# Kernel optimization log

Measured on AMD Instinct MI355X. Metric: run time of the kernel, lower is better.

## Reference

```python
import jax, jax.numpy as jnp
import numpy as np

B, S, D, H = 2, 2048, 1024, 16
DK = D // H


def setup_inputs() -> dict:
    key = jax.random.key(0)
    ks = jax.random.split(key, 11)
    def lin(k):
        kw, kb = jax.random.split(k)
        bound = 1.0 / np.sqrt(D)
        w = jax.random.uniform(kw, (D, D), jnp.float32, -bound, bound)
        b = jax.random.uniform(kb, (D,), jnp.float32, -bound, bound)
        return w, b
    wq_w, wq_b = lin(ks[0])
    wk_w, wk_b = lin(ks[1])
    wv_w, wv_b = lin(ks[2])
    wo_w, wo_b = lin(ks[3])
    q = jax.random.normal(ks[4], (B, S, D), jnp.float32)
    k = jax.random.normal(ks[5], (B, S, D), jnp.float32)
    v = jax.random.normal(ks[6], (B, S, D), jnp.float32)
    # causal mask, broadcastable to (B, H, S, S); 0 -> masked
    mask = jnp.tril(jnp.ones((S, S), jnp.int32))[None, None, :, :]
    return {"q": q, "k": k, "v": v, "mask": mask,
            "wq_w": wq_w, "wq_b": wq_b, "wk_w": wk_w, "wk_b": wk_b,
            "wv_w": wv_w, "wv_b": wv_b, "wo_w": wo_w, "wo_b": wo_b}


def reference(q, k, v, mask, wq_w, wq_b, wk_w, wk_b, wv_w, wv_b, wo_w, wo_b):
    # projections (torch Linear: x @ W^T + b)
    def split_heads(x):  # (B,S,D) -> (B,H,S,DK)
        return x.reshape(B, S, H, DK).transpose(0, 2, 1, 3)
    Q = split_heads(q @ wq_w.T + wq_b)
    K = split_heads(k @ wk_w.T + wk_b)
    V = split_heads(v @ wv_w.T + wv_b)
    scores = jnp.einsum('bhqd,bhkd->bhqk', Q, K) / np.sqrt(DK).astype(np.float32)
    scores = jnp.where(mask == 0, jnp.float32(-1e9), scores)
    attn = jax.nn.softmax(scores, axis=-1)
    out = jnp.einsum('bhqk,bhkd->bhqd', attn, V)  # (B,H,S,DK)
    out = out.transpose(0, 2, 1, 3).reshape(B, S, D)
    return out @ wo_w.T + wo_b
```

## Files before the change

### kernel.cpp

```cpp
#include <hip/hip_runtime.h>

#define DEV __device__ __forceinline__

typedef __attribute__((ext_vector_type(8))) short short8;
typedef __attribute__((ext_vector_type(4))) float f32x4;
typedef __attribute__((ext_vector_type(4))) unsigned int u32x4;
typedef __bf16 bf16x8 __attribute__((ext_vector_type(8)));
typedef unsigned int u32;
typedef unsigned short u16;

constexpr int Bb = 2, Ss = 2048, Dd = 1024, Hh = 16, DKc = 64;
constexpr int Kk = 1024;

#define QSCALE 0.1803368801111204f

DEV u16 f2bf(float f) {
  u32 u = __builtin_bit_cast(u32, f);
  u32 r = (u + 0x7fffu + ((u >> 16) & 1u)) >> 16;
  return (u16)r;
}

DEV u32 pk_bf16(float lo, float hi) {
  u32 w;
  asm("v_cvt_pk_bf16_f32 %0, %1, %2" : "=v"(w) : "v"(lo), "v"(hi));
  return w;
}

DEV f32x4 mfma16(short8 a, short8 b, f32x4 c) {
  return __builtin_amdgcn_mfma_f32_16x16x32_bf16(
      __builtin_bit_cast(bf16x8, a), __builtin_bit_cast(bf16x8, b), c, 0, 0, 0);
}

DEV void gload_lds16(const u16* g, u16* lds) {
  __builtin_amdgcn_global_load_lds(
      (const __attribute__((address_space(1))) u32*)g,
      (__attribute__((address_space(3))) u32*)lds, 16, 0, 0);
}

struct CvtArgs {
  const float* in[4];
  u16* out[4];
  int n[4];
};

__global__ __launch_bounds__(256) void cvt_all(CvtArgs a) {
  int z = blockIdx.z;
  int i = (blockIdx.x * 256 + threadIdx.x) * 4;
  if (i >= a.n[z]) return;
  float4 v = *reinterpret_cast<const float4*>(a.in[z] + i);
  ushort4 o;
  o.x = f2bf(v.x); o.y = f2bf(v.y); o.z = f2bf(v.z); o.w = f2bf(v.w);
  *reinterpret_cast<ushort4*>(a.out[z] + i) = o;
}

template<int MT, int NT>
DEV void gemm_core(const u16* __restrict__ A, const u16* __restrict__ Bt,
                   u16* smA, u16* smB, f32x4 (&acc)[MT][NT], int gm0, int gn0) {
  constexpr int NSTEP = Kk / 32;
  constexpr int SA = MT * 1024;
  constexpr int SB = NT * 1024;
  constexpr int S = MT / 2 + NT / 2;
  const int tid = threadIdx.x;
  const int w = tid >> 6, l = tid & 63;
  const int g = (l >> 4) & 3, r = l & 15;
  const int wm = w >> 1, wn = w & 1;
  const int srow = l >> 2, scol = (l & 3) * 8;

  auto stage = [&](int buf, int kt) {
    int kb = kt * 32;
#pragma unroll
    for (int cc = 0; cc < MT / 2; ++cc) {
      int c = w + cc * 4;
      gload_lds16(A + (size_t)(gm0 + c * 16 + srow) * Kk + kb + scol,
                  smA + buf * SA + c * 512);
    }
#pragma unroll
    for (int cc = 0; cc < NT / 2; ++cc) {
      int c = w + cc * 4;
      gload_lds16(Bt + (size_t)(gn0 + c * 16 + srow) * Kk + kb + scol,
                  smB + buf * SB + c * 512);
    }
  };

  stage(0, 0);
  stage(1, 1);
  for (int kt = 0; kt < NSTEP; ++kt) {
    const int buf = kt % 3;
    if (kt + 1 < NSTEP) {
      if constexpr (S == 4) asm volatile("s_waitcnt vmcnt(4)" ::: "memory");
      else                  asm volatile("s_waitcnt vmcnt(3)" ::: "memory");
    } else {
      asm volatile("s_waitcnt vmcnt(0)" ::: "memory");
    }
    __builtin_amdgcn_s_barrier();
    __builtin_amdgcn_sched_barrier(0);
    if (kt + 2 < NSTEP) stage((kt + 2) % 3, kt + 2);

    short8 af[MT], bf_[NT];
#pragma unroll
    for (int t = 0; t < MT; ++t)
      af[t] = *reinterpret_cast<const short8*>(
          smA + buf * SA + (wm * (MT * 16) + t * 16 + r) * 32 + g * 8);
#pragma unroll
    for (int t = 0; t < NT; ++t)
      bf_[t] = *reinterpret_cast<const short8*>(
          smB + buf * SB + (wn * (NT * 16) + t * 16 + r) * 32 + g * 8);
    __builtin_amdgcn_s_setprio(1);
#pragma unroll
    for (int mt = 0; mt < MT; ++mt)
#pragma unroll
      for (int nt = 0; nt < NT; ++nt)
        acc[mt][nt] = mfma16(af[mt], bf_[nt], acc[mt][nt]);
    __builtin_amdgcn_s_setprio(0);
  }
}

template<int MT, int NT>
DEV void gemm_core_mix(const float* __restrict__ A, const u16* __restrict__ Bt,
                       u16* smA, u16* smB, f32x4 (&acc)[MT][NT], int gm0, int gn0) {
  constexpr int NSTEP = Kk / 32;
  constexpr int SA = MT * 1024, SB = NT * 1024;
  const int tid = threadIdx.x;
  const int w = tid >> 6, l = tid & 63;
  const int g = (l >> 4) & 3, r = l & 15;
  const int wm = w >> 1, wn = w & 1;
  const int srow = l >> 2, scol = (l & 3) * 8;

  float4 a0[MT / 2][2], a1[MT / 2][2];

  auto loadA = [&](float4 (&dst)[MT / 2][2], int kt) {
    int kb = kt * 32;
#pragma unroll
    for (int c = 0; c < MT / 2; ++c) {
      int p = tid + c * 256;
      const float* src = A + (size_t)(gm0 + (p >> 2)) * Kk + kb + (p & 3) * 8;
      dst[c][0] = *reinterpret_cast<const float4*>(src);
      dst[c][1] = *reinterpret_cast<const float4*>(src + 4);
    }
  };
  auto writeA = [&](float4 (&s)[MT / 2][2], int buf) {
#pragma unroll
    for (int c = 0; c < MT / 2; ++c) {
      int p = tid + c * 256;
      u32x4 wv;
      wv.x = pk_bf16(s[c][0].x, s[c][0].y);
      wv.y = pk_bf16(s[c][0].z, s[c][0].w);
      wv.z = pk_bf16(s[c][1].x, s[c][1].y);
      wv.w = pk_bf16(s[c][1].z, s[c][1].w);
      *reinterpret_cast<u32x4*>(smA + buf * SA + p * 8) = wv;
    }
  };
  auto stageB = [&](int buf, int kt) {
    int kb = kt * 32;
#pragma unroll
    for (int cc = 0; cc < NT / 2; ++cc) {
      int c = w + cc * 4;
      gload_lds16(Bt + (size_t)(gn0 + c * 16 + srow) * Kk + kb + scol,
                  smB + buf * SB + c * 512);
    }
  };

  loadA(a0, 0); stageB(0, 0);
  loadA(a1, 1); stageB(1, 1);
  for (int kt = 0; kt < NSTEP; ++kt) {
    const int bufA = kt & 1, bufB = kt % 3;
    if (kt & 1) { writeA(a1, bufA); if (kt + 2 < NSTEP) loadA(a1, kt + 2); }
    else        { writeA(a0, bufA); if (kt + 2 < NSTEP) loadA(a0, kt + 2); }
    if (kt + 2 < NSTEP)      asm volatile("s_waitcnt vmcnt(10)" ::: "memory");
    else if (kt + 1 < NSTEP) asm volatile("s_waitcnt vmcnt(6)" ::: "memory");
    else                     asm volatile("s_waitcnt vmcnt(0)" ::: "memory");
    asm volatile("s_waitcnt lgkmcnt(0)" ::: "memory");
    __builtin_amdgcn_s_barrier();
    __builtin_amdgcn_sched_barrier(0);
    if (kt + 2 < NSTEP) stageB((kt + 2) % 3, kt + 2);

    short8 af[MT], bf_[NT];
#pragma unroll
    for (int t = 0; t < MT; ++t)
      af[t] = *reinterpret_cast<const short8*>(
          smA + bufA * SA + (wm * (MT * 16) + t * 16 + r) * 32 + g * 8);
#pragma unroll
    for (int t = 0; t < NT; ++t)
      bf_[t] = *reinterpret_cast<const short8*>(
          smB + bufB * SB + (wn * (NT * 16) + t * 16 + r) * 32 + g * 8);
    __builtin_amdgcn_s_setprio(1);
#pragma unroll
    for (int mt = 0; mt < MT; ++mt)
#pragma unroll
      for (int nt = 0; nt < NT; ++nt)
        acc[mt][nt] = mfma16(af[mt], bf_[nt], acc[mt][nt]);
    __builtin_amdgcn_s_setprio(0);
  }
}

__global__ __launch_bounds__(256, 3) void proj_qkv(
    const float* __restrict__ xq, const float* __restrict__ xk, const float* __restrict__ xv,
    const u16* __restrict__ Wq, const u16* __restrict__ Wk, const u16* __restrict__ Wv,
    const float* __restrict__ bq, const float* __restrict__ bk, const float* __restrict__ bv,
    u16* __restrict__ Qh, u16* __restrict__ Kh, u16* __restrict__ Vt) {
  __shared__ u16 smA[2 * 4096], smB[3 * 4096];
  const int flat = (blockIdx.z * 32 + blockIdx.y) * 8 + blockIdx.x;
  const int zby = (flat & 7) * 12 + ((flat >> 3) % 12);
  const int bx = flat / 96;
  const int z = zby >> 5, by = zby & 31;
  const float* A = z == 0 ? xq : (z == 1 ? xk : xv);
  const u16* W = z == 0 ? Wq : (z == 1 ? Wk : Wv);
  const float* bias = z == 0 ? bq : (z == 1 ? bk : bv);
  u16* out = z == 0 ? Qh : (z == 1 ? Kh : Vt);
  const float sc = z == 0 ? QSCALE : 1.0f;
  const int gm0 = by * 128, gn0 = bx * 128;
  f32x4 acc[4][4] = {};
  gemm_core_mix<4, 4>(A, W, smA, smB, acc, gm0, gn0);

  const int tid = threadIdx.x;
  const int w = tid >> 6, l = tid & 63, g = (l >> 4) & 3, r = l & 15;
  const int wm = w >> 1, wn = w & 1;
#pragma unroll
  for (int mt = 0; mt < 4; ++mt) {
#pragma unroll
    for (int nt = 0; nt < 4; ++nt) {
      int ncol = gn0 + wn * 64 + nt * 16 + r;
      int h = ncol >> 6, dk = ncol & 63;
      float bb = bias[ncol];
      int mrow0 = gm0 + wm * 64 + mt * 16 + g * 4;
      int b = mrow0 >> 11, s0 = mrow0 & 2047;
      if (z < 2) {
#pragma unroll
        for (int i = 0; i < 4; ++i)
          out[(((size_t)b * Hh + h) * Ss + s0 + i) * DKc + dk] =
              f2bf((acc[mt][nt][i] + bb) * sc);
      } else {
        ushort4 ov;
        ov.x = f2bf(acc[mt][nt][0] + bb);
        ov.y = f2bf(acc[mt][nt][1] + bb);
        ov.z = f2bf(acc[mt][nt][2] + bb);
        ov.w = f2bf(acc[mt][nt][3] + bb);
        *reinterpret_cast<ushort4*>(
            &out[(((size_t)b * Hh + h) * DKc + dk) * Ss + s0]) = ov;
      }
    }
  }
}

__global__ __launch_bounds__(256, 2) void attn(
    const u16* __restrict__ Qh, const u16* __restrict__ Kh,
    const u16* __restrict__ Vt, u16* __restrict__ Ob) {
  __shared__ u16 smK[4][64 * 64];
  __shared__ u16 smV[4][64 * 64];
  __shared__ u16 smP[4][16 * 72];

  const int fid = blockIdx.y * 16 + blockIdx.x;
  const int xcd = fid & 7, slot = fid >> 3;
  const int bh = xcd * 4 + (slot >> 4);
  const int pair = slot & 15;
  const int bidx = bh >> 4, h = bh & 15;

  const int tid = threadIdx.x, w = tid >> 6, l = tid & 63;
  const int g = (l >> 4) & 3, r = l & 15;

  const u16* Qb = Qh + (size_t)bh * Ss * DKc;
  const u16* Kb = Kh + (size_t)bh * Ss * DKc;
  const u16* Vb = Vt + (size_t)bh * DKc * Ss;
  u16* Pw = smP[w];

  const int srow0 = tid >> 3, schunk = tid & 7;

  auto stage = [&](int sl, int kb) {
#pragma unroll
    for (int j = 0; j < 2; ++j) {
      int row = j * 32 + srow0;
      int c = schunk ^ (row & 7);
      u16* dK = smK[sl] + (j * 256 + w * 64) * 8;
      u16* dV = smV[sl] + (j * 256 + w * 64) * 8;
      gload_lds16(Kb + (size_t)(kb + row) * DKc + c * 8, dK);
      gload_lds16(Vb + (size_t)row * Ss + kb + c * 8, dV);
    }
  };

  for (int t2 = 0; t2 < 2; ++t2) {
    const int qt = (t2 == 0) ? (31 - pair) : pair;
    const int ntile = qt + 1;
    const int npair = (ntile + 1) >> 1;
    const int qw = qt * 64 + w * 16;
    const int q = qw + r;

    if (t2) __builtin_amdgcn_s_barrier();

    short8 qf[2];
    qf[0] = *reinterpret_cast<const short8*>(Qb + (size_t)q * DKc + g * 8);
    qf[1] = *reinterpret_cast<const short8*>(Qb + (size_t)q * DKc + 32 + g * 8);

    stage(0, 0);
    if (ntile > 1) stage(1, 64);

    f32x4 o[4] = {};
    float m_s = -3e38f, l_s = 0.f;

    for (int pp = 0; pp < npair; ++pp) {
      const int slotA = (pp & 1) * 2;
      const int kbA = pp * 128;
      const bool hasB = (2 * pp + 1 < ntile);
      const bool diagA = (2 * pp == qt);
      const bool diagB = hasB && (2 * pp + 1 == qt);

      asm volatile("s_waitcnt vmcnt(0)" ::: "memory");
      __builtin_amdgcn_s_barrier();
      __builtin_amdgcn_sched_barrier(0);
      if (pp + 1 < npair) {
        int nb = ((pp + 1) & 1) * 2;
        stage(nb, kbA + 128);
        if (2 * pp + 3 < ntile) stage(nb + 1, kbA + 192);
      }

      f32x4 sA[4] = {}, sB[4] = {};
      __builtin_amdgcn_s_setprio(1);
#pragma unroll
      for (int ks = 0; ks < 2; ++ks)
#pragma unroll
        for (int nt = 0; nt < 4; ++nt) {
          int row = nt * 16 + r;
          int ch = (ks * 4 + g) ^ (row & 7);
          short8 kf = *reinterpret_cast<const short8*>(&smK[slotA][row * 64 + ch * 8]);
          sA[nt] = mfma16(kf, qf[ks], sA[nt]);
        }
      if (hasB) {
#pragma unroll
        for (int ks = 0; ks < 2; ++ks)
#pragma unroll
          for (int nt = 0; nt < 4; ++nt) {
            int row = nt * 16 + r;
            int ch = (ks * 4 + g) ^ (row & 7);
            short8 kf = *reinterpret_cast<const short8*>(&smK[slotA + 1][row * 64 + ch * 8]);
            sB[nt] = mfma16(kf, qf[ks], sB[nt]);
          }
      }
      __builtin_amdgcn_s_setprio(0);

      const int qloc = w * 16 + r;
      if (diagA) {
#pragma unroll
        for (int nt = 0; nt < 4; ++nt)
#pragma unroll
          for (int i = 0; i < 4; ++i)
            if (nt * 16 + g * 4 + i > qloc) sA[nt][i] = -1e30f;
      }
      if (diagB) {
#pragma unroll
        for (int nt = 0; nt < 4; ++nt)
#pragma unroll
          for (int i = 0; i < 4; ++i)
            if (nt * 16 + g * 4 + i > qloc) sB[nt][i] = -1e30f;
      }

      float mx0 = fmaxf(fmaxf(sA[0][0], sA[0][1]), fmaxf(sA[0][2], sA[0][3]));
      float mx1 = fmaxf(fmaxf(sA[1][0], sA[1][1]), fmaxf(sA[1][2], sA[1][3]));
      float mx2 = fmaxf(fmaxf(sA[2][0], sA[2][1]), fmaxf(sA[2][2], sA[2][3]));
      float mx3 = fmaxf(fmaxf(sA[3][0], sA[3][1]), fmaxf(sA[3][2], sA[3][3]));
      float mx = fmaxf(fmaxf(mx0, mx1), fmaxf(mx2, mx3));
      if (hasB) {
        float nx0 = fmaxf(fmaxf(sB[0][0], sB[0][1]), fmaxf(sB[0][2], sB[0][3]));
        float nx1 = fmaxf(fmaxf(sB[1][0], sB[1][1]), fmaxf(sB[1][2], sB[1][3]));
        float nx2 = fmaxf(fmaxf(sB[2][0], sB[2][1]), fmaxf(sB[2][2], sB[2][3]));
        float nx3 = fmaxf(fmaxf(sB[3][0], sB[3][1]), fmaxf(sB[3][2], sB[3][3]));
        mx = fmaxf(mx, fmaxf(fmaxf(nx0, nx1), fmaxf(nx2, nx3)));
      }

      if (__any(mx > m_s + 8.f)) {
        float mr = fmaxf(mx, __shfl_xor(mx, 16));
        mr = fmaxf(mr, __shfl_xor(mr, 32));
        float mn = fmaxf(m_s, mr);
        float f = __builtin_amdgcn_exp2f(m_s - mn);
        m_s = mn;
        l_s *= f;
#pragma unroll
        for (int dt = 0; dt < 4; ++dt) {
          o[dt][0] *= f; o[dt][1] *= f; o[dt][2] *= f; o[dt][3] *= f;
        }
      }

#pragma unroll
      for (int nt = 0; nt < 4; ++nt) {
        float p0 = __builtin_amdgcn_exp2f(sA[nt][0] - m_s);
        float p1 = __builtin_amdgcn_exp2f(sA[nt][1] - m_s);
        float p2 = __builtin_amdgcn_exp2f(sA[nt][2] - m_s);
        float p3 = __builtin_amdgcn_exp2f(sA[nt][3] - m_s);
        l_s += (p0 + p1) + (p2 + p3);
        *reinterpret_cast<u32*>(&Pw[r * 72 + nt * 16 + g * 4])     = pk_bf16(p0, p1);
        *reinterpret_cast<u32*>(&Pw[r * 72 + nt * 16 + g * 4 + 2]) = pk_bf16(p2, p3);
      }
      __builtin_amdgcn_s_setprio(1);
#pragma unroll
      for (int ks = 0; ks < 2; ++ks) {
        short8 pf = *reinterpret_cast<const short8*>(&Pw[r * 72 + ks * 32 + g * 8]);
#pragma unroll
        for (int dt = 0; dt < 4; ++dt) {
          int row = dt * 16 + r;
          int ch = (ks * 4 + g) ^ (row & 7);
          short8 vf = *reinterpret_cast<const short8*>(&smV[slotA][row * 64 + ch * 8]);
          o[dt] = mfma16(vf, pf, o[dt]);
        }
      }
      __builtin_amdgcn_s_setprio(0);

      if (hasB) {
#pragma unroll
        for (int nt = 0; nt < 4; ++nt) {
          float p0 = __builtin_amdgcn_exp2f(sB[nt][0] - m_s);
          float p1 = __builtin_amdgcn_exp2f(sB[nt][1] - m_s);
          float p2 = __builtin_amdgcn_exp2f(sB[nt][2] - m_s);
          float p3 = __builtin_amdgcn_exp2f(sB[nt][3] - m_s);
          l_s += (p0 + p1) + (p2 + p3);
          *reinterpret_cast<u32*>(&Pw[r * 72 + nt * 16 + g * 4])     = pk_bf16(p0, p1);
          *reinterpret_cast<u32*>(&Pw[r * 72 + nt * 16 + g * 4 + 2]) = pk_bf16(p2, p3);
        }
        __builtin_amdgcn_s_setprio(1);
#pragma unroll
        for (int ks = 0; ks < 2; ++ks) {
          short8 pf = *reinterpret_cast<const short8*>(&Pw[r * 72 + ks * 32 + g * 8]);
#pragma unroll
          for (int dt = 0; dt < 4; ++dt) {
            int row = dt * 16 + r;
            int ch = (ks * 4 + g) ^ (row & 7);
            short8 vf = *reinterpret_cast<const short8*>(&smV[slotA + 1][row * 64 + ch * 8]);
            o[dt] = mfma16(vf, pf, o[dt]);
          }
        }
        __builtin_amdgcn_s_setprio(0);
      }
    }

    float lt = l_s;
    lt += __shfl_xor(lt, 16);
    lt += __shfl_xor(lt, 32);
    float inv = 1.f / lt;
    size_t ro = ((size_t)bidx * Ss + q) * Dd + h * DKc;
#pragma unroll
    for (int dt = 0; dt < 4; ++dt) {
      ushort4 ov;
      ov.x = f2bf(o[dt][0] * inv);
      ov.y = f2bf(o[dt][1] * inv);
      ov.z = f2bf(o[dt][2] * inv);
      ov.w = f2bf(o[dt][3] * inv);
      *reinterpret_cast<ushort4*>(&Ob[ro + dt * 16 + g * 4]) = ov;
    }
  }
}

__global__ __launch_bounds__(256, 2) void gemm_out(
    const u16* __restrict__ Ob, const u16* __restrict__ Wo,
    const float* __restrict__ bo, float* __restrict__ out) {
  __shared__ u16 smA[3 * 64 * 32], smB[3 * 128 * 32];
  const int flat = blockIdx.y * 8 + blockIdx.x;
  const int by = (flat & 7) * 8 + ((flat >> 3) & 7);
  const int bx = flat >> 6;
  const int gm0 = by * 64, gn0 = bx * 128;
  f32x4 acc[2][4] = {};
  gemm_core<2, 4>(Ob, Wo, smA, smB, acc, gm0, gn0);

  const int tid = threadIdx.x;
  const int w = tid >> 6, l = tid & 63, g = (l >> 4) & 3, r = l & 15;
  const int wm = w >> 1, wn = w & 1;
#pragma unroll
  for (int mt = 0; mt < 2; ++mt) {
#pragma unroll
    for (int nt = 0; nt < 4; ++nt) {
      int ncol = gn0 + wn * 64 + nt * 16 + r;
      float bb = bo[ncol];
#pragma unroll
      for (int i = 0; i < 4; ++i) {
        int mrow = gm0 + wm * 32 + mt * 16 + g * 4 + i;
        out[(size_t)mrow * Dd + ncol] = acc[mt][nt][i] + bb;
      }
    }
  }
}

extern "C" void kernel_launch(void* const* d_in, const int* in_sizes, int n_in,
                              void* d_out, int out_size, void* d_ws, size_t ws_size,
                              hipStream_t stream) {
  const float* q    = (const float*)d_in[0];
  const float* k    = (const float*)d_in[1];
  const float* v    = (const float*)d_in[2];
  const float* wq_w = (const float*)d_in[4];
  const float* wq_b = (const float*)d_in[5];
  const float* wk_w = (const float*)d_in[6];
  const float* wk_b = (const float*)d_in[7];
  const float* wv_w = (const float*)d_in[8];
  const float* wv_b = (const float*)d_in[9];
  const float* wo_w = (const float*)d_in[10];
  const float* wo_b = (const float*)d_in[11];

  char* ws = (char*)d_ws;
  u16* Wqb = (u16*)(ws + 25165824);
  u16* Wkb = (u16*)(ws + 27262976);
  u16* Wvb = (u16*)(ws + 29360128);
  u16* Wob = (u16*)(ws + 31457280);
  u16* Qh  = (u16*)(ws + 33554432);
  u16* Kh  = (u16*)(ws + 41943040);
  u16* Vt  = (u16*)(ws + 50331648);
  u16* Ob  = (u16*)(ws + 0);

  CvtArgs ca;
  ca.in[0] = wq_w; ca.out[0] = Wqb; ca.n[0] = 1048576;
  ca.in[1] = wk_w; ca.out[1] = Wkb; ca.n[1] = 1048576;
  ca.in[2] = wv_w; ca.out[2] = Wvb; ca.n[2] = 1048576;
  ca.in[3] = wo_w; ca.out[3] = Wob; ca.n[3] = 1048576;

  cvt_all<<<dim3(1024, 1, 4), 256, 0, stream>>>(ca);
  proj_qkv<<<dim3(8, 32, 3), 256, 0, stream>>>(q, k, v, Wqb, Wkb, Wvb,
                                               wq_b, wk_b, wv_b, Qh, Kh, Vt);
  attn<<<dim3(16, 32), 256, 0, stream>>>(Qh, Kh, Vt, Ob);
  gemm_out<<<dim3(8, 64), 256, 0, stream>>>(Ob, Wob, wo_b, (float*)d_out);
}
```

Measured before the change: 109.5 us.

## Split K/V staging, one q-tile per block, unroll GEMM loop by two

The attention kernel now gives each block a single query tile, launches twice as many blocks ordered heaviest first, and drops the paired heavy/light tile balancing and the XCD-aware block mapping. K and V use separate double buffers, so the next K tiles load while softmax and PV run and V is refetched after PV. Shared memory is smaller and launch bounds go to 3 blocks per CU. The padded P stride changes from 72 to 76. The GEMM core loop is unrolled by two with the A register write moved between fragment loads and MFMAs to overlap LDS writes with compute. This risks load imbalance from causal tile sizes and more barriers per iteration.

```diff
diff --git a/kernel.cpp b/kernel.cpp
--- a/kernel.cpp
+++ b/kernel.cpp
@@ -159,37 +159,53 @@
                   smB + buf * SB + c * 512);
     }
   };
+  auto frags = [&](int bufA, int bufB, short8 (&af)[MT], short8 (&bf_)[NT]) {
+#pragma unroll
+    for (int t = 0; t < MT; ++t)
+      af[t] = *reinterpret_cast<const short8*>(
+          smA + bufA * SA + (wm * (MT * 16) + t * 16 + r) * 32 + g * 8);
+#pragma unroll
+    for (int t = 0; t < NT; ++t)
+      bf_[t] = *reinterpret_cast<const short8*>(
+          smB + bufB * SB + (wn * (NT * 16) + t * 16 + r) * 32 + g * 8);
+  };
+  auto mma = [&](short8 (&af)[MT], short8 (&bf_)[NT]) {
+    __builtin_amdgcn_s_setprio(1);
+#pragma unroll
+    for (int mt = 0; mt < MT; ++mt)
+#pragma unroll
+      for (int nt = 0; nt < NT; ++nt)
+        acc[mt][nt] = mfma16(af[mt], bf_[nt], acc[mt][nt]);
+    __builtin_amdgcn_s_setprio(0);
+  };
 
   loadA(a0, 0); stageB(0, 0);
   loadA(a1, 1); stageB(1, 1);
-  for (int kt = 0; kt < NSTEP; ++kt) {
-    const int bufA = kt & 1, bufB = kt % 3;
-    if (kt & 1) { writeA(a1, bufA); if (kt + 2 < NSTEP) loadA(a1, kt + 2); }
-    else        { writeA(a0, bufA); if (kt + 2 < NSTEP) loadA(a0, kt + 2); }
-    if (kt + 2 < NSTEP)      asm volatile("s_waitcnt vmcnt(10)" ::: "memory");
-    else if (kt + 1 < NSTEP) asm volatile("s_waitcnt vmcnt(6)" ::: "memory");
-    else                     asm volatile("s_waitcnt vmcnt(0)" ::: "memory");
+  writeA(a0, 0);
+
+  for (int kt = 0; kt < NSTEP; kt += 2) {
+    asm volatile("s_waitcnt vmcnt(10)" ::: "memory");
     asm volatile("s_waitcnt lgkmcnt(0)" ::: "memory");
     __builtin_amdgcn_s_barrier();
     __builtin_amdgcn_sched_barrier(0);
-    if (kt + 2 < NSTEP) stageB((kt + 2) % 3, kt + 2);
-
-    short8 af[MT], bf_[NT];
-#pragma unroll
-    for (int t = 0; t < MT; ++t)
-      af[t] = *reinterpret_cast<const short8*>(
-          smA + bufA * SA + (wm * (MT * 16) + t * 16 + r) * 32 + g * 8);
-#pragma unroll
-    for (int t = 0; t < NT; ++t)
-      bf_[t] = *reinterpret_cast<const short8*>(
-          smB + bufB * SB + (wn * (NT * 16) + t * 16 + r) * 32 + g * 8);
-    __builtin_amdgcn_s_setprio(1);
-#pragma unroll
-    for (int mt = 0; mt < MT; ++mt)
-#pragma unroll
-      for (int nt = 0; nt < NT; ++nt)
-        acc[mt][nt] = mfma16(af[mt], bf_[nt], acc[mt][nt]);
-    __builtin_amdgcn_s_setprio(0);
+    if (kt + 2 < NSTEP) { stageB((kt + 2) % 3, kt + 2); loadA(a0, kt + 2); }
+    {
+      short8 af[MT], bf_[NT];
+      frags(0, kt % 3, af, bf_);
+      writeA(a1, 1);
+      mma(af, bf_);
+    }
+    asm volatile("s_waitcnt vmcnt(10)" ::: "memory");
+    asm volatile("s_waitcnt lgkmcnt(0)" ::: "memory");
+    __builtin_amdgcn_s_barrier();
+    __builtin_amdgcn_sched_barrier(0);
+    if (kt + 3 < NSTEP) { stageB((kt + 3) % 3, kt + 3); loadA(a1, kt + 3); }
+    {
+      short8 af[MT], bf_[NT];
+      frags(1, (kt + 1) % 3, af, bf_);
+      if (kt + 2 < NSTEP) writeA(a0, 0);
+      mma(af, bf_);
+    }
   }
 }
 
@@ -242,17 +258,15 @@
   }
 }
 
-__global__ __launch_bounds__(256, 2) void attn(
+__global__ __launch_bounds__(256, 3) void attn(
     const u16* __restrict__ Qh, const u16* __restrict__ Kh,
     const u16* __restrict__ Vt, u16* __restrict__ Ob) {
-  __shared__ u16 smK[4][64 * 64];
-  __shared__ u16 smV[4][64 * 64];
-  __shared__ u16 smP[4][16 * 72];
-
-  const int fid = blockIdx.y * 16 + blockIdx.x;
-  const int xcd = fid & 7, slot = fid >> 3;
-  const int bh = xcd * 4 + (slot >> 4);
-  const int pair = slot & 15;
+  __shared__ u16 smK[2][64 * 64];
+  __shared__ u16 smV[2][64 * 64];
+  __shared__ u16 smP[4][16 * 76];
+
+  const int bh = blockIdx.x;
+  const int qt = 31 - blockIdx.y;
   const int bidx = bh >> 4, h = bh & 15;
 
   const int tid = threadIdx.x, w = tid >> 6, l = tid & 63;
@@ -265,184 +279,199 @@
 
   const int srow0 = tid >> 3, schunk = tid & 7;
 
-  auto stage = [&](int sl, int kb) {
+  auto stageK = [&](int sl, int kb) {
 #pragma unroll
     for (int j = 0; j < 2; ++j) {
       int row = j * 32 + srow0;
       int c = schunk ^ (row & 7);
-      u16* dK = smK[sl] + (j * 256 + w * 64) * 8;
-      u16* dV = smV[sl] + (j * 256 + w * 64) * 8;
-      gload_lds16(Kb + (size_t)(kb + row) * DKc + c * 8, dK);
-      gload_lds16(Vb + (size_t)row * Ss + kb + c * 8, dV);
-    }
-  };
-
-  for (int t2 = 0; t2 < 2; ++t2) {
-    const int qt = (t2 == 0) ? (31 - pair) : pair;
-    const int ntile = qt + 1;
-    const int npair = (ntile + 1) >> 1;
-    const int qw = qt * 64 + w * 16;
-    const int q = qw + r;
-
-    if (t2) __builtin_amdgcn_s_barrier();
-
-    short8 qf[2];
-    qf[0] = *reinterpret_cast<const short8*>(Qb + (size_t)q * DKc + g * 8);
-    qf[1] = *reinterpret_cast<const short8*>(Qb + (size_t)q * DKc + 32 + g * 8);
-
-    stage(0, 0);
-    if (ntile > 1) stage(1, 64);
-
-    f32x4 o[4] = {};
-    float m_s = -3e38f, l_s = 0.f;
-
-    for (int pp = 0; pp < npair; ++pp) {
-      const int slotA = (pp & 1) * 2;
-      const int kbA = pp * 128;
-      const bool hasB = (2 * pp + 1 < ntile);
-      const bool diagA = (2 * pp == qt);
-      const bool diagB = hasB && (2 * pp + 1 == qt);
-
-      asm volatile("s_waitcnt vmcnt(0)" ::: "memory");
-      __builtin_amdgcn_s_barrier();
-      __builtin_amdgcn_sched_barrier(0);
-      if (pp + 1 < npair) {
-        int nb = ((pp + 1) & 1) * 2;
-        stage(nb, kbA + 128);
-        if (2 * pp + 3 < ntile) stage(nb + 1, kbA + 192);
-      }
-
-      f32x4 sA[4] = {}, sB[4] = {};
-      __builtin_amdgcn_s_setprio(1);
+      gload_lds16(Kb + (size_t)(kb + row) * DKc + c * 8,
+                  smK[sl] + (j * 256 + w * 64) * 8);
+    }
+  };
+  auto stageV = [&](int sl, int kb) {
+#pragma unroll
+    for (int j = 0; j < 2; ++j) {
+      int row = j * 32 + srow0;
+      int c = schunk ^ (row & 7);
+      gload_lds16(Vb + (size_t)row * Ss + kb + c * 8,
+                  smV[sl] + (j * 256 + w * 64) * 8);
+    }
+  };
+
+  const int ntile = qt + 1;
+  const int npair = (ntile + 1) >> 1;
+  const int qw = qt * 64 + w * 16;
+  const int q = qw + r;
+
+  short8 qf[2];
+  qf[0] = *reinterpret_cast<const short8*>(Qb + (size_t)q * DKc + g * 8);
+  qf[1] = *reinterpret_cast<const short8*>(Qb + (size_t)q * DKc + 32 + g * 8);
+
+  {
+    int kb1 = (ntile > 1) ? 64 : 0;
+    stageK(0, 0); stageK(1, kb1);
+    stageV(0, 0); stageV(1, kb1);
+  }
+
+  f32x4 o[4] = {};
+  float m_s = -3e38f, l_s = 0.f;
+
+  for (int pp = 0; pp < npair; ++pp) {
+    const int kbA = pp * 128;
+    const bool hasB = (2 * pp + 1 < ntile);
+    const bool diagA = (2 * pp == qt);
+    const bool diagB = hasB && (2 * pp + 1 == qt);
+
+    asm volatile("s_waitcnt vmcnt(4)" ::: "memory");
+    __builtin_amdgcn_s_barrier();
+    __builtin_amdgcn_sched_barrier(0);
+
+    f32x4 sA[4] = {}, sB[4] = {};
+    __builtin_amdgcn_s_setprio(1);
+#pragma unroll
+    for (int ks = 0; ks < 2; ++ks)
+#pragma unroll
+      for (int nt = 0; nt < 4; ++nt) {
+        int row = nt * 16 + r;
+        int ch = (ks * 4 + g) ^ (row & 7);
+        short8 kf = *reinterpret_cast<const short8*>(&smK[0][row * 64 + ch * 8]);
+        sA[nt] = mfma16(kf, qf[ks], sA[nt]);
+      }
+    if (hasB) {
 #pragma unroll
       for (int ks = 0; ks < 2; ++ks)
 #pragma unroll
         for (int nt = 0; nt < 4; ++nt) {
           int row = nt * 16 + r;
           int ch = (ks * 4 + g) ^ (row & 7);
-          short8 kf = *reinterpret_cast<const short8*>(&smK[slotA][row * 64 + ch * 8]);
-          sA[nt] = mfma16(kf, qf[ks], sA[nt]);
+          short8 kf = *reinterpret_cast<const short8*>(&smK[1][row * 64 + ch * 8]);
+          sB[nt] = mfma16(kf, qf[ks], sB[nt]);
         }
-      if (hasB) {
-#pragma unroll
-        for (int ks = 0; ks < 2; ++ks)
-#pragma unroll
-          for (int nt = 0; nt < 4; ++nt) {
-            int row = nt * 16 + r;
-            int ch = (ks * 4 + g) ^ (row & 7);
-            short8 kf = *reinterpret_cast<const short8*>(&smK[slotA + 1][row * 64 + ch * 8]);
-            sB[nt] = mfma16(kf, qf[ks], sB[nt]);
-          }
-      }
-      __builtin_amdgcn_s_setprio(0);
-
-      const int qloc = w * 16 + r;
-      if (diagA) {
-#pragma unroll
-        for (int nt = 0; nt < 4; ++nt)
-#pragma unroll
-          for (int i = 0; i < 4; ++i)
-            if (nt * 16 + g * 4 + i > qloc) sA[nt][i] = -1e30f;
-      }
-      if (diagB) {
-#pragma unroll
-        for (int nt = 0; nt < 4; ++nt)
-#pragma unroll
-          for (int i = 0; i < 4; ++i)
-            if (nt * 16 + g * 4 + i > qloc) sB[nt][i] = -1e30f;
-      }
-
-      float mx0 = fmaxf(fmaxf(sA[0][0], sA[0][1]), fmaxf(sA[0][2], sA[0][3]));
-      float mx1 = fmaxf(fmaxf(sA[1][0], sA[1][1]), fmaxf(sA[1][2], sA[1][3]));
-      float mx2 = fmaxf(fmaxf(sA[2][0], sA[2][1]), fmaxf(sA[2][2], sA[2][3]));
-      float mx3 = fmaxf(fmaxf(sA[3][0], sA[3][1]), fmaxf(sA[3][2], sA[3][3]));
-      float mx = fmaxf(fmaxf(mx0, mx1), fmaxf(mx2, mx3));
-      if (hasB) {
-        float nx0 = fmaxf(fmaxf(sB[0][0], sB[0][1]), fmaxf(sB[0][2], sB[0][3]));
-        float nx1 = fmaxf(fmaxf(sB[1][0], sB[1][1]), fmaxf(sB[1][2], sB[1][3]));
-        float nx2 = fmaxf(fmaxf(sB[2][0], sB[2][1]), fmaxf(sB[2][2], sB[2][3]));
-        float nx3 = fmaxf(fmaxf(sB[3][0], sB[3][1]), fmaxf(sB[3][2], sB[3][3]));
-        mx = fmaxf(mx, fmaxf(fmaxf(nx0, nx1), fmaxf(nx2, nx3)));
-      }
-
-      if (__any(mx > m_s + 8.f)) {
-        float mr = fmaxf(mx, __shfl_xor(mx, 16));
-        mr = fmaxf(mr, __shfl_xor(mr, 32));
-        float mn = fmaxf(m_s, mr);
-        float f = __builtin_amdgcn_exp2f(m_s - mn);
-        m_s = mn;
-        l_s *= f;
-#pragma unroll
-        for (int dt = 0; dt < 4; ++dt) {
-          o[dt][0] *= f; o[dt][1] *= f; o[dt][2] *= f; o[dt][3] *= f;
-        }
-      }
-
+    }
+    __builtin_amdgcn_s_setprio(0);
+
+    asm volatile("s_waitcnt vmcnt(0)" ::: "memory");
+    __builtin_amdgcn_s_barrier();
+    __builtin_amdgcn_sched_barrier(0);
+    if (pp + 1 < npair) {
+      int nkb = kbA + 128;
+      int nkb1 = (2 * pp + 3 < ntile) ? nkb + 64 : nkb;
+      stageK(0, nkb); stageK(1, nkb1);
+    }
+
+    const int qloc = w * 16 + r;
+    if (diagA) {
+#pragma unroll
+      for (int nt = 0; nt < 4; ++nt)
+#pragma unroll
+        for (int i = 0; i < 4; ++i)
+          if (nt * 16 + g * 4 + i > qloc) sA[nt][i] = -1e30f;
+    }
+    if (diagB) {
+#pragma unroll
+      for (int nt = 0; nt < 4; ++nt)
+#pragma unroll
+        for (int i = 0; i < 4; ++i)
+          if (nt * 16 + g * 4 + i > qloc) sB[nt][i] = -1e30f;
+    }
+
+    float mx0 = fmaxf(fmaxf(sA[0][0], sA[0][1]), fmaxf(sA[0][2], sA[0][3]));
+    float mx1 = fmaxf(fmaxf(sA[1][0], sA[1][1]), fmaxf(sA[1][2], sA[1][3]));
+    float mx2 = fmaxf(fmaxf(sA[2][0], sA[2][1]), fmaxf(sA[2][2], sA[2][3]));
+    float mx3 = fmaxf(fmaxf(sA[3][0], sA[3][1]), fmaxf(sA[3][2], sA[3][3]));
+    float mx = fmaxf(fmaxf(mx0, mx1), fmaxf(mx2, mx3));
+    if (hasB) {
+      float nx0 = fmaxf(fmaxf(sB[0][0], sB[0][1]), fmaxf(sB[0][2], sB[0][3]));
+      float nx1 = fmaxf(fmaxf(sB[1][0], sB[1][1]), fmaxf(sB[1][2], sB[1][3]));
+      float nx2 = fmaxf(fmaxf(sB[2][0], sB[2][1]), fmaxf(sB[2][2], sB[2][3]));
+      float nx3 = fmaxf(fmaxf(sB[3][0], sB[3][1]), fmaxf(sB[3][2], sB[3][3]));
+      mx = fmaxf(mx, fmaxf(fmaxf(nx0, nx1), fmaxf(nx2, nx3)));
+    }
+
+    if (__any(mx > m_s + 8.f)) {
+      float mr = fmaxf(mx, __shfl_xor(mx, 16));
+      mr = fmaxf(mr, __shfl_xor(mr, 32));
+      float mn = fmaxf(m_s, mr);
+      float f = __builtin_amdgcn_exp2f(m_s - mn);
+      m_s = mn;
+      l_s *= f;
+#pragma unroll
+      for (int dt = 0; dt < 4; ++dt) {
+        o[dt][0] *= f; o[dt][1] *= f; o[dt][2] *= f; o[dt][3] *= f;
+      }
+    }
+
+#pragma unroll
+    for (int nt = 0; nt < 4; ++nt) {
+      float p0 = __builtin_amdgcn_exp2f(sA[nt][0] - m_s);
+      float p1 = __builtin_amdgcn_exp2f(sA[nt][1] - m_s);
+      float p2 = __builtin_amdgcn_exp2f(sA[nt][2] - m_s);
+      float p3 = __builtin_amdgcn_exp2f(sA[nt][3] - m_s);
+      l_s += (p0 + p1) + (p2 + p3);
+      *reinterpret_cast<u32*>(&Pw[r * 76 + nt * 16 + g * 4])     = pk_bf16(p0, p1);
+      *reinterpret_cast<u32*>(&Pw[r * 76 + nt * 16 + g * 4 + 2]) = pk_bf16(p2, p3);
+    }
+    __builtin_amdgcn_s_setprio(1);
+#pragma unroll
+    for (int ks = 0; ks < 2; ++ks) {
+      short8 pf = *reinterpret_cast<const short8*>(&Pw[r * 76 + ks * 32 + g * 8]);
+#pragma unroll
+      for (int dt = 0; dt < 4; ++dt) {
+        int row = dt * 16 + r;
+        int ch = (ks * 4 + g) ^ (row & 7);
+        short8 vf = *reinterpret_cast<const short8*>(&smV[0][row * 64 + ch * 8]);
+        o[dt] = mfma16(vf, pf, o[dt]);
+      }
+    }
+    __builtin_amdgcn_s_setprio(0);
+
+    if (hasB) {
 #pragma unroll
       for (int nt = 0; nt < 4; ++nt) {
-        float p0 = __builtin_amdgcn_exp2f(sA[nt][0] - m_s);
-        float p1 = __builtin_amdgcn_exp2f(sA[nt][1] - m_s);
-        float p2 = __builtin_amdgcn_exp2f(sA[nt][2] - m_s);
-        float p3 = __builtin_amdgcn_exp2f(sA[nt][3] - m_s);
+        float p0 = __builtin_amdgcn_exp2f(sB[nt][0] - m_s);
+        float p1 = __builtin_amdgcn_exp2f(sB[nt][1] - m_s);
+        float p2 = __builtin_amdgcn_exp2f(sB[nt][2] - m_s);
+        float p3 = __builtin_amdgcn_exp2f(sB[nt][3] - m_s);
         l_s += (p0 + p1) + (p2 + p3);
-        *reinterpret_cast<u32*>(&Pw[r * 72 + nt * 16 + g * 4])     = pk_bf16(p0, p1);
-        *reinterpret_cast<u32*>(&Pw[r * 72 + nt * 16 + g * 4 + 2]) = pk_bf16(p2, p3);
+        *reinterpret_cast<u32*>(&Pw[r * 76 + nt * 16 + g * 4])     = pk_bf16(p0, p1);
+        *reinterpret_cast<u32*>(&Pw[r * 76 + nt * 16 + g * 4 + 2]) = pk_bf16(p2, p3);
       }
       __builtin_amdgcn_s_setprio(1);
 #pragma unroll
       for (int ks = 0; ks < 2; ++ks) {
-        short8 pf = *reinterpret_cast<const short8*>(&Pw[r * 72 + ks * 32 + g * 8]);
+        short8 pf = *reinterpret_cast<const short8*>(&Pw[r * 76 + ks * 32 + g * 8]);
 #pragma unroll
         for (int dt = 0; dt < 4; ++dt) {
           int row = dt * 16 + r;
           int ch = (ks * 4 + g) ^ (row & 7);
-          short8 vf = *reinterpret_cast<const short8*>(&smV[slotA][row * 64 + ch * 8]);
+          short8 vf = *reinterpret_cast<const short8*>(&smV[1][row * 64 + ch * 8]);
           o[dt] = mfma16(vf, pf, o[dt]);
         }
       }
       __builtin_amdgcn_s_setprio(0);
-
-      if (hasB) {
-#pragma unroll
-        for (int nt = 0; nt < 4; ++nt) {
-          float p0 = __builtin_amdgcn_exp2f(sB[nt][0] - m_s);
-          float p1 = __builtin_amdgcn_exp2f(sB[nt][1] - m_s);
-          float p2 = __builtin_amdgcn_exp2f(sB[nt][2] - m_s);
-          float p3 = __builtin_amdgcn_exp2f(sB[nt][3] - m_s);
-          l_s += (p0 + p1) + (p2 + p3);
-          *reinterpret_cast<u32*>(&Pw[r * 72 + nt * 16 + g * 4])     = pk_bf16(p0, p1);
-          *reinterpret_cast<u32*>(&Pw[r * 72 + nt * 16 + g * 4 + 2]) = pk_bf16(p2, p3);
-        }
-        __builtin_amdgcn_s_setprio(1);
-#pragma unroll
-        for (int ks = 0; ks < 2; ++ks) {
-          short8 pf = *reinterpret_cast<const short8*>(&Pw[r * 72 + ks * 32 + g * 8]);
-#pragma unroll
-          for (int dt = 0; dt < 4; ++dt) {
-            int row = dt * 16 + r;
-            int ch = (ks * 4 + g) ^ (row & 7);
-            short8 vf = *reinterpret_cast<const short8*>(&smV[slotA + 1][row * 64 + ch * 8]);
-            o[dt] = mfma16(vf, pf, o[dt]);
-          }
-        }
-        __builtin_amdgcn_s_setprio(0);
-      }
-    }
-
-    float lt = l_s;
-    lt += __shfl_xor(lt, 16);
-    lt += __shfl_xor(lt, 32);
-    float inv = 1.f / lt;
-    size_t ro = ((size_t)bidx * Ss + q) * Dd + h * DKc;
-#pragma unroll
-    for (int dt = 0; dt < 4; ++dt) {
-      ushort4 ov;
-      ov.x = f2bf(o[dt][0] * inv);
-      ov.y = f2bf(o[dt][1] * inv);
-      ov.z = f2bf(o[dt][2] * inv);
-      ov.w = f2bf(o[dt][3] * inv);
-      *reinterpret_cast<ushort4*>(&Ob[ro + dt * 16 + g * 4]) = ov;
-    }
+    }
+
+    __builtin_amdgcn_s_barrier();
+    if (pp + 1 < npair) {
+      int nkb = kbA + 128;
+      int nkb1 = (2 * pp + 3 < ntile) ? nkb + 64 : nkb;
+      stageV(0, nkb); stageV(1, nkb1);
+    }
+  }
+
+  float lt = l_s;
+  lt += __shfl_xor(lt, 16);
+  lt += __shfl_xor(lt, 32);
+  float inv = 1.f / lt;
+  size_t ro = ((size_t)bidx * Ss + q) * Dd + h * DKc;
+#pragma unroll
+  for (int dt = 0; dt < 4; ++dt) {
+    ushort4 ov;
+    ov.x = f2bf(o[dt][0] * inv);
+    ov.y = f2bf(o[dt][1] * inv);
+    ov.z = f2bf(o[dt][2] * inv);
+    ov.w = f2bf(o[dt][3] * inv);
+    *reinterpret_cast<ushort4*>(&Ob[ro + dt * 16 + g * 4]) = ov;
   }
 }
 
@@ -509,6 +538,6 @@
   cvt_all<<<dim3(1024, 1, 4), 256, 0, stream>>>(ca);
   proj_qkv<<<dim3(8, 32, 3), 256, 0, stream>>>(q, k, v, Wqb, Wkb, Wvb,
                                                wq_b, wk_b, wv_b, Qh, Kh, Vt);
-  attn<<<dim3(16, 32), 256, 0, stream>>>(Qh, Kh, Vt, Ob);
+  attn<<<dim3(32, 32), 256, 0, stream>>>(Qh, Kh, Vt, Ob);
   gemm_out<<<dim3(8, 64), 256, 0, stream>>>(Ob, Wob, wo_b, (float*)d_out);
 }
```

Measured after the change: 115.0 us. +5.1%, slower.
